# Kernel tuning notes

Hardware: AMD Instinct MI355X
Metric: run time of the kernel (lower is better)

The kernel has to match this reference:

```python
import jax, jax.numpy as jnp
import numpy as np

B, S, D, O = 1, 2048, 512, 512
H, QD, K, PK = 8, 256, 16, 256
N = PK * PK  # 65536 experts
HALF = QD // 2  # sub-query dim per product-key dimension


def _l2norm(x):
    # matches F.normalize(dim=-1): x / max(||x||, 1e-12)
    n = jnp.sqrt(jnp.sum(x * x, axis=-1, keepdims=True))
    return x / jnp.maximum(n, 1e-12)


def setup_inputs() -> dict:
    key = jax.random.key(0)
    ks = jax.random.split(key, 9)
    return {
        "hidden_states": jax.random.normal(ks[0], (B, S, D), jnp.float32),
        "Wq": jax.random.normal(ks[1], (H * QD, D), jnp.float32) * 0.02,
        "bq": jnp.zeros((H * QD,), jnp.float32),
        "ln_g": jnp.ones((QD,), jnp.float32),
        "ln_b": jnp.zeros((QD,), jnp.float32),
        "keys0": jax.random.normal(ks[2], (PK, HALF), jnp.float32) * 0.02,
        "keys1": jax.random.normal(ks[3], (PK, HALF), jnp.float32) * 0.02,
        "expert_down": jax.random.normal(ks[4], (N, D), jnp.float32) * 0.02,
        "expert_up": jax.random.normal(ks[5], (N, O), jnp.float32) * 0.02,
    }


def reference(hidden_states, Wq, bq, ln_g, ln_b, keys0, keys1, expert_down, expert_up):
    b, s, d = hidden_states.shape
    # query projection + layernorm over query_dim
    q = (hidden_states @ Wq.T + bq).reshape(b, s, H, QD)
    mu = jnp.mean(q, axis=-1, keepdims=True)
    var = jnp.mean((q - mu) ** 2, axis=-1, keepdims=True)
    q = (q - mu) / jnp.sqrt(var + 1e-5) * ln_g + ln_b
    # split into per-dimension sub-queries, normalize queries and keys
    q0, q1 = q[..., :HALF], q[..., HALF:]
    s0 = jnp.einsum('bshq,eq->bshe', _l2norm(q0), _l2norm(keys0))  # [b,s,H,PK]
    s1 = jnp.einsum('bshq,eq->bshe', _l2norm(q1), _l2norm(keys1))
    # per-dim top-k' (k' = K=16 here due to clamping logic in source)
    sc0, ix0 = jax.lax.top_k(s0, K)
    sc1, ix1 = jax.lax.top_k(s1, K)
    # combinatorial merge: scores add; NOTE source adds indices with multiplier 1
    # for the last dim and never scales the first-dim indices (faithful repro).
    cs = (sc0[..., :, None] + sc1[..., None, :]).reshape(b, s, H, K * K)
    ci = (ix0[..., :, None] + ix1[..., None, :]).reshape(b, s, H, K * K)
    fs, pos = jax.lax.top_k(cs, K)
    fi = jnp.take_along_axis(ci, pos, axis=-1)  # [b,s,H,K] expert ids
    w = jax.nn.softmax(fs, axis=-1)
    # gather rank-1 experts and apply: down-project, gelu, up-project, combine
    down = expert_down[fi]  # [b,s,H,K,D]
    up = expert_up[fi]      # [b,s,H,K,O]
    inner = jnp.einsum('bsd,bshkd->bshk', hidden_states, down)
    act = jax.nn.gelu(inner, approximate=False)
    out = jnp.einsum('bshk,bshko->bso', act * w, up)
    return out
```

## Files before the change

kernel.cpp:

```cpp
#include <hip/hip_runtime.h>
#include <math.h>

constexpr int Sx    = 2048;
constexpr int Dx    = 512;
constexpr int Hx    = 8;
constexpr int QDx   = 256;
constexpr int HALFx = 128;
constexpr int PKx   = 256;
constexpr int Kx    = 16;
constexpr int HQx   = Hx * QDx;
constexpr int Rx    = Sx * Hx;
constexpr int Ox    = 512;

__global__ __launch_bounds__(64) void knorm_kernel(
    const float* __restrict__ k0, const float* __restrict__ k1,
    float* __restrict__ k0n, float* __restrict__ k1n)
{
    const int row = blockIdx.x;
    const float* src = (row < PKx) ? (k0 + (size_t)row * HALFx)
                                   : (k1 + (size_t)(row - PKx) * HALFx);
    float* dst = (row < PKx) ? (k0n + (size_t)row * HALFx)
                             : (k1n + (size_t)(row - PKx) * HALFx);
    const int t = threadIdx.x;
    float a = src[t];
    float b = src[t + 64];
    float ss = a * a + b * b;
#pragma unroll
    for (int off = 32; off; off >>= 1) ss += __shfl_xor(ss, off);
    float n = sqrtf(ss);
    n = fmaxf(n, 1e-12f);
    dst[t]      = a / n;
    dst[t + 64] = b / n;
}

__global__ __launch_bounds__(256) void qproj_kernel(
    const float* __restrict__ A,
    const float* __restrict__ W,
    const float* __restrict__ bq,
    float* __restrict__ C)
{
    constexpr int BM = 64, BN = 64, BK = 32, PAD = 4;
    __shared__ __align__(16) float As[BK][BM + PAD];
    __shared__ __align__(16) float Bs[BK][BN + PAD];
    const int bm = blockIdx.y * BM;
    const int bn = blockIdx.x * BN;
    const int tid = threadIdx.x;
    const int tx = tid & 15;
    const int ty = tid >> 4;
    float acc[4][4] = {{0.f}};
    for (int k0 = 0; k0 < Dx; k0 += BK) {
#pragma unroll
        for (int i = 0; i < (BM * BK) / 256; ++i) {
            int idx = tid + i * 256;
            int m = idx >> 5;
            int k = idx & 31;
            As[k][m] = A[(size_t)(bm + m) * Dx + k0 + k];
            Bs[k][m] = W[(size_t)(bn + m) * Dx + k0 + k];
        }
        __syncthreads();
#pragma unroll
        for (int k = 0; k < BK; ++k) {
            float4 av = *(const float4*)&As[k][ty * 4];
            float4 bv = *(const float4*)&Bs[k][tx * 4];
            float a4[4] = {av.x, av.y, av.z, av.w};
            float b4[4] = {bv.x, bv.y, bv.z, bv.w};
#pragma unroll
            for (int i = 0; i < 4; ++i)
#pragma unroll
                for (int j = 0; j < 4; ++j)
                    acc[i][j] = fmaf(a4[i], b4[j], acc[i][j]);
        }
        __syncthreads();
    }
#pragma unroll
    for (int i = 0; i < 4; ++i) {
        const int row = bm + ty * 4 + i;
#pragma unroll
        for (int j = 0; j < 4; ++j) {
            const int col = bn + tx * 4 + j;
            C[(size_t)row * HQx + col] = acc[i][j] + bq[col];
        }
    }
}

__global__ __launch_bounds__(64) void ln_kernel(
    float* __restrict__ q, const float* __restrict__ g,
    const float* __restrict__ b)
{
    const int r = blockIdx.x;
    float* row = q + (size_t)r * QDx;
    const int t = threadIdx.x;
    float v0 = row[t], v1 = row[t + 64], v2 = row[t + 128], v3 = row[t + 192];
    float sum = v0 + v1 + v2 + v3;
#pragma unroll
    for (int off = 32; off; off >>= 1) sum += __shfl_xor(sum, off);
    const float mu = sum * (1.f / 256.f);
    float d0 = v0 - mu, d1 = v1 - mu, d2 = v2 - mu, d3 = v3 - mu;
    float ss = d0 * d0 + d1 * d1 + d2 * d2 + d3 * d3;
#pragma unroll
    for (int off = 32; off; off >>= 1) ss += __shfl_xor(ss, off);
    const float var = ss * (1.f / 256.f);
    const float inv = 1.0f / sqrtf(var + 1e-5f);
    v0 = d0 * inv * g[t]       + b[t];
    v1 = d1 * inv * g[t + 64]  + b[t + 64];
    v2 = d2 * inv * g[t + 128] + b[t + 128];
    v3 = d3 * inv * g[t + 192] + b[t + 192];
    float s0 = v0 * v0 + v1 * v1;
#pragma unroll
    for (int off = 32; off; off >>= 1) s0 += __shfl_xor(s0, off);
    float n0 = fmaxf(sqrtf(s0), 1e-12f);
    float s1 = v2 * v2 + v3 * v3;
#pragma unroll
    for (int off = 32; off; off >>= 1) s1 += __shfl_xor(s1, off);
    float n1 = fmaxf(sqrtf(s1), 1e-12f);
    row[t]       = v0 / n0;
    row[t + 64]  = v1 / n0;
    row[t + 128] = v2 / n1;
    row[t + 192] = v3 / n1;
}

__global__ __launch_bounds__(256) void score_kernel(
    const float* __restrict__ qn,
    const float* __restrict__ k0n, const float* __restrict__ k1n,
    float* __restrict__ s0, float* __restrict__ s1)
{
    constexpr int BM = 64, BN = 64, BK = 32, PAD = 4;
    __shared__ __align__(16) float As[BK][BM + PAD];
    __shared__ __align__(16) float Bs[BK][BN + PAD];
    const int half = blockIdx.z;
    const float* B = half ? k1n : k0n;
    float* Sout = half ? s1 : s0;
    const int bm = blockIdx.y * BM;
    const int bn = blockIdx.x * BN;
    const int tid = threadIdx.x;
    const int tx = tid & 15;
    const int ty = tid >> 4;
    const int coff = half * HALFx;
    float acc[4][4] = {{0.f}};
    for (int k0 = 0; k0 < HALFx; k0 += BK) {
#pragma unroll
        for (int i = 0; i < (BM * BK) / 256; ++i) {
            int idx = tid + i * 256;
            int m = idx >> 5;
            int k = idx & 31;
            As[k][m] = qn[(size_t)(bm + m) * QDx + coff + k0 + k];
            Bs[k][m] = B[(size_t)(bn + m) * HALFx + k0 + k];
        }
        __syncthreads();
#pragma unroll
        for (int k = 0; k < BK; ++k) {
            float4 av = *(const float4*)&As[k][ty * 4];
            float4 bv = *(const float4*)&Bs[k][tx * 4];
            float a4[4] = {av.x, av.y, av.z, av.w};
            float b4[4] = {bv.x, bv.y, bv.z, bv.w};
#pragma unroll
            for (int i = 0; i < 4; ++i)
#pragma unroll
                for (int j = 0; j < 4; ++j)
                    acc[i][j] = fmaf(a4[i], b4[j], acc[i][j]);
        }
        __syncthreads();
    }
#pragma unroll
    for (int i = 0; i < 4; ++i)
#pragma unroll
        for (int j = 0; j < 4; ++j)
            Sout[(size_t)(bm + ty * 4 + i) * PKx + bn + tx * 4 + j] = acc[i][j];
}

__device__ __forceinline__ unsigned fkey(float f) {
    unsigned u = __float_as_uint(f);
    return u ^ ((u & 0x80000000u) ? 0xFFFFFFFFu : 0x80000000u);
}

__device__ __forceinline__ void extract16(
    const float v[4], const unsigned u[4], unsigned T, int lane,
    unsigned long long lmask, float* outv, int* outi)
{
    unsigned long long mg[4];
    int gt_total = 0;
#pragma unroll
    for (int j = 0; j < 4; ++j) {
        mg[j] = __ballot(u[j] > T);
        gt_total += __popcll(mg[j]);
    }
    int bg = 0, be = gt_total;
#pragma unroll
    for (int j = 0; j < 4; ++j) {
        unsigned long long me = __ballot(u[j] == T);
        int idx = lane + 64 * j;
        if (u[j] > T) {
            int pg = bg + __popcll(mg[j] & lmask);
            outv[pg] = v[j]; outi[pg] = idx;
        } else if (u[j] == T) {
            int pe = be + __popcll(me & lmask);
            if (pe < 16) { outv[pe] = v[j]; outi[pe] = idx; }
        }
        bg += __popcll(mg[j]);
        be += __popcll(me);
    }
}

__global__ __launch_bounds__(64) void topk_kernel(
    const float* __restrict__ s0g, const float* __restrict__ s1g,
    int* __restrict__ fib, float* __restrict__ wb)
{
    __shared__ float sc0[Kx], sc1[Kx], fsv[Kx];
    __shared__ int ix0[Kx], ix1[Kx], fid[Kx];
    const int r = blockIdx.x;
    const int lane = threadIdx.x;
    const unsigned long long lmask = (1ull << lane) - 1ull;

    float v0[4], v1[4];
    unsigned u0[4], u1[4];
#pragma unroll
    for (int j = 0; j < 4; ++j) {
        v0[j] = s0g[(size_t)r * PKx + lane + 64 * j];
        v1[j] = s1g[(size_t)r * PKx + lane + 64 * j];
        u0[j] = fkey(v0[j]);
        u1[j] = fkey(v1[j]);
    }

    unsigned T0 = 0, T1 = 0;
    for (int bit = 31; bit >= 0; --bit) {
        const unsigned c0 = T0 | (1u << bit);
        const unsigned c1 = T1 | (1u << bit);
        int n0 = 0, n1 = 0;
#pragma unroll
        for (int j = 0; j < 4; ++j) {
            n0 += __popcll(__ballot(u0[j] >= c0));
            n1 += __popcll(__ballot(u1[j] >= c1));
        }
        if (n0 >= Kx) T0 = c0;
        if (n1 >= Kx) T1 = c1;
    }
    extract16(v0, u0, T0, lane, lmask, sc0, ix0);
    extract16(v1, u1, T1, lane, lmask, sc1, ix1);
    __syncthreads();

    float cv[4];
    unsigned cu[4];
    int ci[4];
#pragma unroll
    for (int j = 0; j < 4; ++j) {
        int p = lane + 64 * j;
        cv[j] = sc0[p >> 4] + sc1[p & 15];
        cu[j] = fkey(cv[j]);
        ci[j] = ix0[p >> 4] + ix1[p & 15];
    }
    unsigned T2 = 0;
    for (int bit = 31; bit >= 0; --bit) {
        const unsigned c2 = T2 | (1u << bit);
        int n2 = 0;
#pragma unroll
        for (int j = 0; j < 4; ++j) n2 += __popcll(__ballot(cu[j] >= c2));
        if (n2 >= Kx) T2 = c2;
    }
    {
        unsigned long long mg[4];
        int gt_total = 0;
#pragma unroll
        for (int j = 0; j < 4; ++j) {
            mg[j] = __ballot(cu[j] > T2);
            gt_total += __popcll(mg[j]);
        }
        int bg = 0, be = gt_total;
#pragma unroll
        for (int j = 0; j < 4; ++j) {
            unsigned long long me = __ballot(cu[j] == T2);
            if (cu[j] > T2) {
                int pg = bg + __popcll(mg[j] & lmask);
                fsv[pg] = cv[j]; fid[pg] = ci[j];
            } else if (cu[j] == T2) {
                int pe = be + __popcll(me & lmask);
                if (pe < 16) { fsv[pe] = cv[j]; fid[pe] = ci[j]; }
            }
            bg += __popcll(mg[j]);
            be += __popcll(me);
        }
    }
    __syncthreads();

    float f = fsv[lane & 15];
    float mx = f;
#pragma unroll
    for (int off = 8; off; off >>= 1) mx = fmaxf(mx, __shfl_xor(mx, off, 16));
    float e = expf(f - mx);
    float sum = e;
#pragma unroll
    for (int off = 8; off; off >>= 1) sum += __shfl_xor(sum, off, 16);
    if (lane < Kx) {
        fib[(size_t)r * Kx + lane] = fid[lane];
        wb[(size_t)r * Kx + lane]  = e / sum;
    }
}

__global__ __launch_bounds__(256) void expert_kernel(
    const float* __restrict__ hidden, const float* __restrict__ down,
    const float* __restrict__ up, const int* __restrict__ fib,
    const float* __restrict__ wb, float* __restrict__ out)
{
    __shared__ float hs[Dx];
    __shared__ float aw[Hx * Kx];
    __shared__ int fis[Hx * Kx];
    const int s = blockIdx.x;
    const int tid = threadIdx.x;
    hs[tid]       = hidden[(size_t)s * Dx + tid];
    hs[tid + 256] = hidden[(size_t)s * Dx + tid + 256];
    if (tid < Hx * Kx) fis[tid] = fib[(size_t)s * (Hx * Kx) + tid];
    __syncthreads();
    const int wv = tid >> 6;
    const int lane = tid & 63;
    for (int p = wv; p < Hx * Kx; p += 4) {
        const float* dr = down + (size_t)fis[p] * Dx;
        float acc = 0.f;
#pragma unroll
        for (int i = 0; i < 8; ++i)
            acc = fmaf(hs[lane + 64 * i], dr[lane + 64 * i], acc);
#pragma unroll
        for (int off = 32; off; off >>= 1) acc += __shfl_xor(acc, off);
        if (lane == 0) {
            float x = acc;
            float act = 0.5f * x * (1.f + erff(x * 0.70710678118654752f));
            aw[p] = act * wb[(size_t)s * (Hx * Kx) + p];
        }
    }
    __syncthreads();
    float a0 = 0.f, a1 = 0.f;
    for (int p = 0; p < Hx * Kx; ++p) {
        const float a = aw[p];
        const float* ur = up + (size_t)fis[p] * Ox;
        a0 = fmaf(a, ur[tid], a0);
        a1 = fmaf(a, ur[tid + 256], a1);
    }
    out[(size_t)s * Ox + tid]       = a0;
    out[(size_t)s * Ox + tid + 256] = a1;
}

extern "C" void kernel_launch(void* const* d_in, const int* in_sizes, int n_in,
                              void* d_out, int out_size, void* d_ws, size_t ws_size,
                              hipStream_t stream)
{
    const float* hidden = (const float*)d_in[0];
    const float* Wq     = (const float*)d_in[1];
    const float* bq     = (const float*)d_in[2];
    const float* ln_g   = (const float*)d_in[3];
    const float* ln_b   = (const float*)d_in[4];
    const float* keys0  = (const float*)d_in[5];
    const float* keys1  = (const float*)d_in[6];
    const float* edown  = (const float*)d_in[7];
    const float* eup    = (const float*)d_in[8];
    float* out = (float*)d_out;

    float* ws  = (float*)d_ws;
    float* q   = ws;
    float* k0n = q + (size_t)Sx * HQx;
    float* k1n = k0n + (size_t)PKx * HALFx;
    float* s0  = k1n + (size_t)PKx * HALFx;
    float* s1  = s0 + (size_t)Rx * PKx;
    float* wb  = s1 + (size_t)Rx * PKx;
    int*   fib = (int*)(wb + (size_t)Rx * Kx);

    hipLaunchKernelGGL(knorm_kernel, dim3(2 * PKx), dim3(64), 0, stream,
                       keys0, keys1, k0n, k1n);
    hipLaunchKernelGGL(qproj_kernel, dim3(HQx / 64, Sx / 64), dim3(256), 0, stream,
                       hidden, Wq, bq, q);
    hipLaunchKernelGGL(ln_kernel, dim3(Rx), dim3(64), 0, stream, q, ln_g, ln_b);
    hipLaunchKernelGGL(score_kernel, dim3(PKx / 64, Rx / 64, 2), dim3(256), 0, stream,
                       q, k0n, k1n, s0, s1);
    hipLaunchKernelGGL(topk_kernel, dim3(Rx), dim3(64), 0, stream, s0, s1, fib, wb);
    hipLaunchKernelGGL(expert_kernel, dim3(Sx), dim3(256), 0, stream,
                       hidden, edown, eup, fib, wb, out);
}
```

Before: 407.2 us.

## Unify GEMMs into register-prefetched 128x64 tiled kernel and vectorize expert up-projection

Replaces the separate query-projection and score GEMMs with one generic 128x64-tile kernel. It uses 8x4 per-thread register tiles, float4 global loads and a register prefetch of the next K-slice that overlaps the shared-memory compute. The score GEMM is now issued as two launches, one per half. The expert kernel keeps hidden values in registers and splits the up-projection across waves, with float4 loads and a shared-memory reduction of the partial sums. The intent is higher arithmetic intensity and better memory coalescing, in exchange for more registers and an extra launch.

Result: slower. 429.5 us (+5.5%).

```diff
diff --git a/kernel.cpp b/kernel.cpp
--- a/kernel.cpp
+++ b/kernel.cpp
@@ -33,53 +33,85 @@
     dst[t + 64] = b / n;
 }
 
-__global__ __launch_bounds__(256) void qproj_kernel(
-    const float* __restrict__ A,
-    const float* __restrict__ W,
-    const float* __restrict__ bq,
-    float* __restrict__ C)
-{
-    constexpr int BM = 64, BN = 64, BK = 32, PAD = 4;
-    __shared__ __align__(16) float As[BK][BM + PAD];
-    __shared__ __align__(16) float Bs[BK][BN + PAD];
+__global__ __launch_bounds__(256) void gemm128_kernel(
+    const float* __restrict__ A, int lda,
+    const float* __restrict__ B, int ldb,
+    const float* __restrict__ bias,
+    float* __restrict__ C, int ldc, int K)
+{
+    constexpr int BM = 128, BN = 64, BK = 32;
+    constexpr int ASTR = BM + 4;
+    constexpr int BSTR = BN + 4;
+    __shared__ __align__(16) float As[BK * ASTR];
+    __shared__ __align__(16) float Bs[BK * BSTR];
+    const int tid = threadIdx.x;
     const int bm = blockIdx.y * BM;
     const int bn = blockIdx.x * BN;
-    const int tid = threadIdx.x;
-    const int tx = tid & 15;
-    const int ty = tid >> 4;
-    float acc[4][4] = {{0.f}};
-    for (int k0 = 0; k0 < Dx; k0 += BK) {
-#pragma unroll
-        for (int i = 0; i < (BM * BK) / 256; ++i) {
-            int idx = tid + i * 256;
-            int m = idx >> 5;
-            int k = idx & 31;
-            As[k][m] = A[(size_t)(bm + m) * Dx + k0 + k];
-            Bs[k][m] = W[(size_t)(bn + m) * Dx + k0 + k];
-        }
+
+    const int sq = tid & 7;
+    const int sr = tid >> 3;
+    const int m0 = (tid >> 4) * 8;
+    const int n0 = (tid & 15) * 4;
+
+    float4 pa[4], pb[2];
+#pragma unroll
+    for (int i = 0; i < 4; ++i)
+        pa[i] = *(const float4*)&A[(size_t)(bm + sr + i * 32) * lda + sq * 4];
+#pragma unroll
+    for (int i = 0; i < 2; ++i)
+        pb[i] = *(const float4*)&B[(size_t)(bn + sr + i * 32) * ldb + sq * 4];
+
+    float acc[8][4] = {{0.f}};
+    const int niter = K / BK;
+    for (int it = 0; it < niter; ++it) {
         __syncthreads();
 #pragma unroll
+        for (int i = 0; i < 4; ++i) {
+            const float v[4] = {pa[i].x, pa[i].y, pa[i].z, pa[i].w};
+#pragma unroll
+            for (int j = 0; j < 4; ++j)
+                As[(sq * 4 + j) * ASTR + sr + i * 32] = v[j];
+        }
+#pragma unroll
+        for (int i = 0; i < 2; ++i) {
+            const float v[4] = {pb[i].x, pb[i].y, pb[i].z, pb[i].w};
+#pragma unroll
+            for (int j = 0; j < 4; ++j)
+                Bs[(sq * 4 + j) * BSTR + sr + i * 32] = v[j];
+        }
+        __syncthreads();
+        if (it + 1 < niter) {
+            const int ko = (it + 1) * BK;
+#pragma unroll
+            for (int i = 0; i < 4; ++i)
+                pa[i] = *(const float4*)&A[(size_t)(bm + sr + i * 32) * lda + ko + sq * 4];
+#pragma unroll
+            for (int i = 0; i < 2; ++i)
+                pb[i] = *(const float4*)&B[(size_t)(bn + sr + i * 32) * ldb + ko + sq * 4];
+        }
+#pragma unroll
         for (int k = 0; k < BK; ++k) {
-            float4 av = *(const float4*)&As[k][ty * 4];
-            float4 bv = *(const float4*)&Bs[k][tx * 4];
-            float a4[4] = {av.x, av.y, av.z, av.w};
-            float b4[4] = {bv.x, bv.y, bv.z, bv.w};
-#pragma unroll
-            for (int i = 0; i < 4; ++i)
+            float af[8], bf[4];
+            *(float4*)&af[0] = *(const float4*)&As[k * ASTR + m0];
+            *(float4*)&af[4] = *(const float4*)&As[k * ASTR + m0 + 4];
+            *(float4*)&bf[0] = *(const float4*)&Bs[k * BSTR + n0];
+#pragma unroll
+            for (int i = 0; i < 8; ++i)
 #pragma unroll
                 for (int j = 0; j < 4; ++j)
-                    acc[i][j] = fmaf(a4[i], b4[j], acc[i][j]);
-        }
-        __syncthreads();
-    }
-#pragma unroll
-    for (int i = 0; i < 4; ++i) {
-        const int row = bm + ty * 4 + i;
-#pragma unroll
-        for (int j = 0; j < 4; ++j) {
-            const int col = bn + tx * 4 + j;
-            C[(size_t)row * HQx + col] = acc[i][j] + bq[col];
-        }
+                    acc[i][j] = fmaf(af[i], bf[j], acc[i][j]);
+        }
+    }
+    float4 bv = make_float4(0.f, 0.f, 0.f, 0.f);
+    if (bias) bv = *(const float4*)&bias[bn + n0];
+#pragma unroll
+    for (int i = 0; i < 8; ++i) {
+        float4 o;
+        o.x = acc[i][0] + bv.x;
+        o.y = acc[i][1] + bv.y;
+        o.z = acc[i][2] + bv.z;
+        o.w = acc[i][3] + bv.w;
+        *(float4*)&C[(size_t)(bm + m0 + i) * ldc + bn + n0] = o;
     }
 }
 
@@ -117,55 +149,6 @@
     row[t + 64]  = v1 / n0;
     row[t + 128] = v2 / n1;
     row[t + 192] = v3 / n1;
-}
-
-__global__ __launch_bounds__(256) void score_kernel(
-    const float* __restrict__ qn,
-    const float* __restrict__ k0n, const float* __restrict__ k1n,
-    float* __restrict__ s0, float* __restrict__ s1)
-{
-    constexpr int BM = 64, BN = 64, BK = 32, PAD = 4;
-    __shared__ __align__(16) float As[BK][BM + PAD];
-    __shared__ __align__(16) float Bs[BK][BN + PAD];
-    const int half = blockIdx.z;
-    const float* B = half ? k1n : k0n;
-    float* Sout = half ? s1 : s0;
-    const int bm = blockIdx.y * BM;
-    const int bn = blockIdx.x * BN;
-    const int tid = threadIdx.x;
-    const int tx = tid & 15;
-    const int ty = tid >> 4;
-    const int coff = half * HALFx;
-    float acc[4][4] = {{0.f}};
-    for (int k0 = 0; k0 < HALFx; k0 += BK) {
-#pragma unroll
-        for (int i = 0; i < (BM * BK) / 256; ++i) {
-            int idx = tid + i * 256;
-            int m = idx >> 5;
-            int k = idx & 31;
-            As[k][m] = qn[(size_t)(bm + m) * QDx + coff + k0 + k];
-            Bs[k][m] = B[(size_t)(bn + m) * HALFx + k0 + k];
-        }
-        __syncthreads();
-#pragma unroll
-        for (int k = 0; k < BK; ++k) {
-            float4 av = *(const float4*)&As[k][ty * 4];
-            float4 bv = *(const float4*)&Bs[k][tx * 4];
-            float a4[4] = {av.x, av.y, av.z, av.w};
-            float b4[4] = {bv.x, bv.y, bv.z, bv.w};
-#pragma unroll
-            for (int i = 0; i < 4; ++i)
-#pragma unroll
-                for (int j = 0; j < 4; ++j)
-                    acc[i][j] = fmaf(a4[i], b4[j], acc[i][j]);
-        }
-        __syncthreads();
-    }
-#pragma unroll
-    for (int i = 0; i < 4; ++i)
-#pragma unroll
-        for (int j = 0; j < 4; ++j)
-            Sout[(size_t)(bm + ty * 4 + i) * PKx + bn + tx * 4 + j] = acc[i][j];
 }
 
 __device__ __forceinline__ unsigned fkey(float f) {
@@ -300,23 +283,24 @@
     const float* __restrict__ up, const int* __restrict__ fib,
     const float* __restrict__ wb, float* __restrict__ out)
 {
-    __shared__ float hs[Dx];
     __shared__ float aw[Hx * Kx];
     __shared__ int fis[Hx * Kx];
+    __shared__ float part[4][Ox];
     const int s = blockIdx.x;
     const int tid = threadIdx.x;
-    hs[tid]       = hidden[(size_t)s * Dx + tid];
-    hs[tid + 256] = hidden[(size_t)s * Dx + tid + 256];
-    if (tid < Hx * Kx) fis[tid] = fib[(size_t)s * (Hx * Kx) + tid];
-    __syncthreads();
     const int wv = tid >> 6;
     const int lane = tid & 63;
+    if (tid < Hx * Kx) fis[tid] = fib[(size_t)s * (Hx * Kx) + tid];
+    float h8[8];
+#pragma unroll
+    for (int i = 0; i < 8; ++i) h8[i] = hidden[(size_t)s * Dx + lane + 64 * i];
+    __syncthreads();
     for (int p = wv; p < Hx * Kx; p += 4) {
         const float* dr = down + (size_t)fis[p] * Dx;
         float acc = 0.f;
 #pragma unroll
         for (int i = 0; i < 8; ++i)
-            acc = fmaf(hs[lane + 64 * i], dr[lane + 64 * i], acc);
+            acc = fmaf(h8[i], dr[lane + 64 * i], acc);
 #pragma unroll
         for (int off = 32; off; off >>= 1) acc += __shfl_xor(acc, off);
         if (lane == 0) {
@@ -326,15 +310,26 @@
         }
     }
     __syncthreads();
-    float a0 = 0.f, a1 = 0.f;
-    for (int p = 0; p < Hx * Kx; ++p) {
+    float a8[8] = {0.f, 0.f, 0.f, 0.f, 0.f, 0.f, 0.f, 0.f};
+    const int o0 = lane * 8;
+    for (int p = wv * 32; p < wv * 32 + 32; ++p) {
         const float a = aw[p];
-        const float* ur = up + (size_t)fis[p] * Ox;
-        a0 = fmaf(a, ur[tid], a0);
-        a1 = fmaf(a, ur[tid + 256], a1);
-    }
-    out[(size_t)s * Ox + tid]       = a0;
-    out[(size_t)s * Ox + tid + 256] = a1;
+        const float* ur = up + (size_t)fis[p] * Ox + o0;
+        float4 u0 = *(const float4*)ur;
+        float4 u1 = *(const float4*)(ur + 4);
+        a8[0] = fmaf(a, u0.x, a8[0]); a8[1] = fmaf(a, u0.y, a8[1]);
+        a8[2] = fmaf(a, u0.z, a8[2]); a8[3] = fmaf(a, u0.w, a8[3]);
+        a8[4] = fmaf(a, u1.x, a8[4]); a8[5] = fmaf(a, u1.y, a8[5]);
+        a8[6] = fmaf(a, u1.z, a8[6]); a8[7] = fmaf(a, u1.w, a8[7]);
+    }
+    *(float4*)&part[wv][o0]     = make_float4(a8[0], a8[1], a8[2], a8[3]);
+    *(float4*)&part[wv][o0 + 4] = make_float4(a8[4], a8[5], a8[6], a8[7]);
+    __syncthreads();
+    float r0 = part[0][tid] + part[1][tid] + part[2][tid] + part[3][tid];
+    float r1 = part[0][tid + 256] + part[1][tid + 256]
+             + part[2][tid + 256] + part[3][tid + 256];
+    out[(size_t)s * Ox + tid]       = r0;
+    out[(size_t)s * Ox + tid + 256] = r1;
 }
 
 extern "C" void kernel_launch(void* const* d_in, const int* in_sizes, int n_in,
@@ -363,11 +358,13 @@
 
     hipLaunchKernelGGL(knorm_kernel, dim3(2 * PKx), dim3(64), 0, stream,
                        keys0, keys1, k0n, k1n);
-    hipLaunchKernelGGL(qproj_kernel, dim3(HQx / 64, Sx / 64), dim3(256), 0, stream,
-                       hidden, Wq, bq, q);
+    hipLaunchKernelGGL(gemm128_kernel, dim3(HQx / 64, Sx / 128), dim3(256), 0, stream,
+                       hidden, Dx, Wq, Dx, bq, q, HQx, Dx);
     hipLaunchKernelGGL(ln_kernel, dim3(Rx), dim3(64), 0, stream, q, ln_g, ln_b);
-    hipLaunchKernelGGL(score_kernel, dim3(PKx / 64, Rx / 64, 2), dim3(256), 0, stream,
-                       q, k0n, k1n, s0, s1);
+    hipLaunchKernelGGL(gemm128_kernel, dim3(PKx / 64, Rx / 128), dim3(256), 0, stream,
+                       q, QDx, k0n, HALFx, (const float*)nullptr, s0, PKx, HALFx);
+    hipLaunchKernelGGL(gemm128_kernel, dim3(PKx / 64, Rx / 128), dim3(256), 0, stream,
+                       q + HALFx, QDx, k1n, HALFx, (const float*)nullptr, s1, PKx, HALFx);
     hipLaunchKernelGGL(topk_kernel, dim3(Rx), dim3(64), 0, stream, s0, s1, fib, wb);
     hipLaunchKernelGGL(expert_kernel, dim3(Sx), dim3(256), 0, stream,
                        hidden, edown, eup, fib, wb, out);
```
